# Optimization experiments

Hardware: AMD Instinct MI355X
Metric: run time of the kernel (lower is better)

## Reference

```python
import jax, jax.numpy as jnp
import numpy as np

NUM_EXPERTS = 8
TOP_K = 2
TOKENS = 4096
HIDDEN = 1024
INTER = 2048
INIT_STD = 0.01  # nnx.initializers.normal() default stddev


def setup_inputs() -> dict:
    key = jax.random.key(0)
    k1, k2, k3, k4, k5 = jax.random.split(key, 5)
    return {
        "inputs": jax.random.normal(k1, (TOKENS, HIDDEN), jnp.float32),
        "router_logits": jax.random.normal(k2, (TOKENS, NUM_EXPERTS), jnp.float32),
        "wi_0": jax.random.normal(k3, (NUM_EXPERTS, HIDDEN, INTER), jnp.float32) * INIT_STD,
        "wi_1": jax.random.normal(k4, (NUM_EXPERTS, HIDDEN, INTER), jnp.float32) * INIT_STD,
        "wo": jax.random.normal(k5, (NUM_EXPERTS, INTER, HIDDEN), jnp.float32) * INIT_STD,
    }


def reference(inputs, router_logits, wi_0, wi_1, wo):
    T, H = inputs.shape
    # --- top-k routing ---
    top_k_logits, top_k_indices = jax.lax.top_k(router_logits, TOP_K)  # [T, k]
    w = jax.nn.softmax(top_k_logits, axis=-1)
    w = w / jnp.sum(w, axis=-1, keepdims=True)  # (redundant renorm, kept faithful)
    # --- permute: sort token-expert pairs by expert id ---
    flat_experts = top_k_indices.reshape(-1)          # [T*k]
    sort_idx = jnp.argsort(flat_experts)              # stable sort -> token order within group
    token_idx = sort_idx // TOP_K                     # source token of each sorted slot
    x = inputs[token_idx]                             # [T*k, H] gathered/permuted tokens
    group_sizes = jnp.bincount(flat_experts, length=NUM_EXPERTS).astype(jnp.int32)
    # --- grouped (ragged) GEMM experts: silu(x@wi_0) * (x@wi_1) @ wo ---
    h0 = jax.lax.ragged_dot(x, wi_0, group_sizes, preferred_element_type=jnp.float32)
    h1 = jax.lax.ragged_dot(x, wi_1, group_sizes, preferred_element_type=jnp.float32)
    act = jax.nn.silu(h0) * h1                        # [T*k, INTER]
    y = jax.lax.ragged_dot(act, wo, group_sizes, preferred_element_type=jnp.float32)  # [T*k, H]
    # --- unpermute + weighted combine over top-k ---
    unsort = jnp.argsort(sort_idx)
    y = y[unsort].reshape(T, TOP_K, H)
    return jnp.sum(y * w[..., None], axis=1)          # [T, H]
```

## Files before the change

kernel.cpp:

```cpp
#include <hip/hip_runtime.h>
#include <hip/hip_bf16.h>

#define T_TOKENS 4096
#define HID 1024
#define INTER 2048
#define NEXP 8
#define TOPK 2
#define RTOT (T_TOKENS * TOPK)
#define BMT 128
#define BN 128
#define MAXT (RTOT / BMT + NEXP)

typedef __attribute__((ext_vector_type(8))) short bf16x8;
typedef __attribute__((ext_vector_type(4))) float f32x4;

typedef __attribute__((address_space(1))) const unsigned int gu32;
typedef __attribute__((address_space(3))) unsigned int lu32;

__device__ __forceinline__ void gl16(const void* g, void* l) {
  __builtin_amdgcn_global_load_lds((gu32*)g, (lu32*)l, 16, 0, 0);
}

__device__ __forceinline__ unsigned f2bf(float f) {
  union { float f; unsigned u; } v; v.f = f;
  unsigned u = v.u;
  return (u + 0x7FFFu + ((u >> 16) & 1u)) >> 16;
}

__device__ __forceinline__ float bf2f(unsigned short s) {
  union { unsigned u; float f; } v; v.u = ((unsigned)s) << 16;
  return v.f;
}

__device__ __forceinline__ int swz(int row, int kb) {
  return row * 128 + (kb ^ ((row & 7) << 4));
}

__device__ __forceinline__ void phase_barrier() {
  asm volatile("" ::: "memory");
  __builtin_amdgcn_s_barrier();
  asm volatile("" ::: "memory");
}

__device__ __forceinline__ int psig(int kap) { return kap ^ ((kap & 1) << 2); }

__global__ __launch_bounds__(1024)
void k_routing(const float* __restrict__ logits, int* ntiles,
               int* te2, int* tr02, int* tcnt2,
               float* pw, int* rows, float* rw, int* slotOf) {
  __shared__ int cnt[NEXP];
  __shared__ int cur[NEXP];
  const int tid = threadIdx.x;
  if (tid < NEXP) cnt[tid] = 0;
  __syncthreads();

  int myE[4][2];
  float myW[4][2];
#pragma unroll
  for (int j = 0; j < 4; ++j) {
    int t = j * 1024 + tid;
    float l[NEXP];
#pragma unroll
    for (int i = 0; i < NEXP; ++i) l[i] = logits[t * NEXP + i];
    int i0 = 0; float b0 = l[0];
#pragma unroll
    for (int i = 1; i < NEXP; ++i) if (l[i] > b0) { b0 = l[i]; i0 = i; }
    int i1 = -1; float b1 = -1e30f;
#pragma unroll
    for (int i = 0; i < NEXP; ++i) if (i != i0 && l[i] > b1) { b1 = l[i]; i1 = i; }
    float e = __expf(b1 - b0);
    float w0 = 1.f / (1.f + e);
    float w1 = e / (1.f + e);
    myE[j][0] = i0; myE[j][1] = i1;
    myW[j][0] = w0; myW[j][1] = w1;
    pw[2 * t] = w0; pw[2 * t + 1] = w1;
#pragma unroll
    for (int ex = 0; ex < NEXP; ++ex) {
      int c = __popcll(__ballot(i0 == ex)) + __popcll(__ballot(i1 == ex));
      if ((tid & 63) == 0 && c) atomicAdd(&cnt[ex], c);
    }
  }
  __syncthreads();

  if (tid == 0) {
    int off = 0, nm = 0;
    for (int e = 0; e < NEXP; ++e) {
      int c = cnt[e];
      cur[e] = off;
      for (int m0 = 0; m0 < c; m0 += BMT) {
        te2[nm] = e; tr02[nm] = off + m0; tcnt2[nm] = min(BMT, c - m0); ++nm;
      }
      off += c;
    }
    ntiles[1] = nm;
  }
  __syncthreads();

#pragma unroll
  for (int j = 0; j < 4; ++j) {
    int t = j * 1024 + tid;
#pragma unroll
    for (int k = 0; k < TOPK; ++k) {
      int e = myE[j][k];
      int s = atomicAdd(&cur[e], 1);
      rows[s] = t;
      rw[s] = myW[j][k];
      slotOf[2 * t + k] = s;
    }
  }
}

__global__ __launch_bounds__(256)
void k_prep1(const float* __restrict__ X, unsigned short* __restrict__ Xb,
             const float* __restrict__ W0, const float* __restrict__ W1,
             unsigned short* __restrict__ T0, unsigned short* __restrict__ T1) {
  int bid = blockIdx.x;
  const int tid = threadIdx.x;
  if (bid < 1024) {
    int base = bid * 1024 + tid;
#pragma unroll
    for (int j = 0; j < 4; ++j) {
      int i = base + j * 256;
      float4 v = *(const float4*)(X + (size_t)i * 4);
      uint2 p;
      p.x = f2bf(v.x) | (f2bf(v.y) << 16);
      p.y = f2bf(v.z) | (f2bf(v.w) << 16);
      *(uint2*)(Xb + (size_t)i * 4) = p;
    }
    return;
  }
  bid -= 1024;
  const int w = bid >> 11;
  const int r = bid & 2047;
  const float* W = (w == 0) ? W0 : W1;
  unsigned short* T = (w == 0) ? T0 : T1;
  const int kt = r & 15, nt = (r >> 4) & 15, e = r >> 8;
  __shared__ float ls[64 * 128];
  const float* src = W + (size_t)e * HID * INTER + (size_t)(kt * 64) * INTER + nt * 128;
#pragma unroll
  for (int t = 0; t < 8; ++t) {
    int u = t * 256 + tid;
    int k = u >> 5, n4 = u & 31;
    float4 v = *(const float4*)(src + (size_t)k * INTER + n4 * 4);
    *(float4*)(ls + k * 128 + ((n4 ^ psig(k >> 3)) << 2)) = v;
  }
  __syncthreads();
  unsigned short* dst = T + (((size_t)e * 16 + nt) * 16 + kt) * 8192;
#pragma unroll
  for (int t = 0; t < 4; ++t) {
    int v = t * 256 + tid;
    int kt2 = v >> 9, n = (v >> 2) & 127, sw = v & 3;
    int kc = kt2 * 4 + (sw ^ ((n >> 1) & 3));
    const float* col = ls + (size_t)(kc * 8) * 128 +
                       (((n >> 2) ^ psig(kc)) << 2) + (n & 3);
    unsigned b[8];
#pragma unroll
    for (int i = 0; i < 8; ++i) b[i] = f2bf(col[i * 128]);
    uint4 q;
    q.x = b[0] | (b[1] << 16); q.y = b[2] | (b[3] << 16);
    q.z = b[4] | (b[5] << 16); q.w = b[6] | (b[7] << 16);
    *(uint4*)(dst + (size_t)v * 8) = q;
  }
}

__global__ __launch_bounds__(512, 4)
void k_gemm1w(const unsigned short* __restrict__ Xb,
              const unsigned short* __restrict__ WT0,
              const unsigned short* __restrict__ WT1,
              const float* __restrict__ WO,
              unsigned short* __restrict__ WTo,
              const int* __restrict__ ntiles, const int* __restrict__ te2,
              const int* __restrict__ tr02, const int* __restrict__ tcnt2,
              const int* __restrict__ rows,
              unsigned short* __restrict__ act) {
  const int ty = blockIdx.y;
  const int nt = blockIdx.x;
  const int tid = threadIdx.x;
  __shared__ __align__(16) unsigned char sm[49152];

  if (ty >= MAXT) {
    const int r = (ty - MAXT) * 16 + nt;
    const int kt = r & 31, ntt = (r >> 5) & 7, e = r >> 8;
    float* ls = (float*)sm;
    const float* src = WO + (size_t)e * INTER * HID + (size_t)(kt * 64) * HID + ntt * 128;
#pragma unroll
    for (int t = 0; t < 4; ++t) {
      int u = t * 512 + tid;
      int k = u >> 5, n4 = u & 31;
      float4 v = *(const float4*)(src + (size_t)k * HID + n4 * 4);
      *(float4*)(ls + k * 128 + ((n4 ^ psig(k >> 3)) << 2)) = v;
    }
    __syncthreads();
    unsigned short* dst = WTo + (((size_t)e * 8 + ntt) * 32 + kt) * 8192;
#pragma unroll
    for (int t = 0; t < 2; ++t) {
      int v = t * 512 + tid;
      int kt2 = v >> 9, n = (v >> 2) & 127, sw = v & 3;
      int kc = kt2 * 4 + (sw ^ ((n >> 1) & 3));
      const float* col = ls + (size_t)(kc * 8) * 128 +
                         (((n >> 2) ^ psig(kc)) << 2) + (n & 3);
      unsigned b[8];
#pragma unroll
      for (int i = 0; i < 8; ++i) b[i] = f2bf(col[i * 128]);
      uint4 q;
      q.x = b[0] | (b[1] << 16); q.y = b[2] | (b[3] << 16);
      q.z = b[4] | (b[5] << 16); q.w = b[6] | (b[7] << 16);
      *(uint4*)(dst + (size_t)v * 8) = q;
    }
    return;
  }

  if (ty >= ntiles[1]) return;
  const int e = te2[ty], row0 = tr02[ty], mcnt = tcnt2[ty];
  const int n0 = nt * BN;
  const int lane = tid & 63, wv = tid >> 6;
  const int mh = wv >> 2, nq = wv & 3;
  const int l15 = lane & 15, sl = lane >> 4;

  const int am = tid >> 2;
  const int atok = rows[row0 + (am < mcnt ? am : mcnt - 1)];
  const int askc = ((tid & 3) ^ ((tid >> 3) & 3)) * 8;
  const unsigned short* B0t = WT0 + ((size_t)e * 16 + nt) * 32 * 4096;
  const unsigned short* B1t = WT1 + ((size_t)e * 16 + nt) * 32 * 4096;

  int aoff[4], boff[2];
#pragma unroll
  for (int f = 0; f < 4; ++f) {
    int m = mh * 64 + f * 16 + l15;
    aoff[f] = m * 64 + ((sl ^ ((m >> 1) & 3)) << 4);
  }
#pragma unroll
  for (int g = 0; g < 2; ++g) {
    int n = nq * 32 + g * 16 + l15;
    boff[g] = n * 64 + ((sl ^ ((n >> 1) & 3)) << 4);
  }

  f32x4 acc0[4][2], acc1[4][2];
  const f32x4 zz = {0.f, 0.f, 0.f, 0.f};
#pragma unroll
  for (int f = 0; f < 4; ++f)
#pragma unroll
    for (int g = 0; g < 2; ++g) { acc0[f][g] = zz; acc1[f][g] = zz; }

  const int NT_K = HID / 32;

  gl16(Xb + (size_t)atok * HID + askc, sm + tid * 16);
  gl16(B0t + (size_t)tid * 8, sm + 8192 + tid * 16);
  gl16(B1t + (size_t)tid * 8, sm + 16384 + tid * 16);

  for (int t = 0; t < NT_K; ++t) {
    unsigned char* cur = sm + (t & 1) * 24576;
    unsigned char* nxt = sm + ((t + 1) & 1) * 24576;
    const int tn = (t + 1 < NT_K) ? (t + 1) : (NT_K - 1);

    gl16(Xb + (size_t)atok * HID + tn * 32 + askc, nxt + tid * 16);
    gl16(B0t + (size_t)tn * 4096 + tid * 8, nxt + 8192 + tid * 16);
    gl16(B1t + (size_t)tn * 4096 + tid * 8, nxt + 16384 + tid * 16);
    asm volatile("s_waitcnt vmcnt(3)" ::: "memory");
    __builtin_amdgcn_sched_barrier(0);
    phase_barrier();

    bf16x8 aA[4], b0q[2], b1q[2];
#pragma unroll
    for (int g = 0; g < 2; ++g) {
      b0q[g] = *(const bf16x8*)(cur + 8192 + boff[g]);
      b1q[g] = *(const bf16x8*)(cur + 16384 + boff[g]);
    }
#pragma unroll
    for (int f = 0; f < 4; ++f) aA[f] = *(const bf16x8*)(cur + aoff[f]);
    __builtin_amdgcn_s_setprio(1);
#pragma unroll
    for (int f = 0; f < 4; ++f)
#pragma unroll
      for (int g = 0; g < 2; ++g) {
        acc0[f][g] = __builtin_amdgcn_mfma_f32_16x16x32_bf16(aA[f], b0q[g], acc0[f][g], 0, 0, 0);
        acc1[f][g] = __builtin_amdgcn_mfma_f32_16x16x32_bf16(aA[f], b1q[g], acc1[f][g], 0, 0, 0);
      }
    __builtin_amdgcn_s_setprio(0);
    phase_barrier();
  }

#pragma unroll
  for (int f = 0; f < 4; ++f) {
#pragma unroll
    for (int r = 0; r < 4; ++r) {
      int m = mh * 64 + f * 16 + sl * 4 + r;
      if (m >= mcnt) continue;
      size_t base = (size_t)(row0 + m) * INTER + n0 + nq * 32 + l15;
#pragma unroll
      for (int g = 0; g < 2; ++g) {
        float h0 = acc0[f][g][r];
        float h1 = acc1[f][g][r];
        float s = h0 / (1.f + __expf(-h0));
        act[base + g * 16] = (unsigned short)f2bf(s * h1);
      }
    }
  }
}

__global__ __launch_bounds__(256, 4)
void k_gemm2n(const unsigned short* __restrict__ act,
              const unsigned short* __restrict__ WTo,
              const int* __restrict__ ntiles, const int* __restrict__ te2,
              const int* __restrict__ tr02, const int* __restrict__ tcnt2,
              unsigned short* __restrict__ y) {
  const int ty = blockIdx.y;
  if (ty >= ntiles[1]) return;
  const int e = te2[ty], row0 = tr02[ty], mcnt = tcnt2[ty];
  const int nt = blockIdx.x, n0 = nt * BN;
  const int tid = threadIdx.x, lane = tid & 63, wv = tid >> 6;
  const int wr = wv >> 1, wc = wv & 1;
  const int l15 = lane & 15, sl = lane >> 4;

  __shared__ __align__(16) unsigned char sm[32768];

  const int am0 = tid >> 2, am1 = 64 + (tid >> 2);
  const int ar0 = row0 + (am0 < mcnt ? am0 : mcnt - 1);
  const int ar1 = row0 + (am1 < mcnt ? am1 : mcnt - 1);
  const int askc = ((tid & 3) ^ ((tid >> 3) & 3)) * 8;
  const unsigned short* Bt = WTo + ((size_t)e * 8 + nt) * 64 * 4096;

  int aoff[4], boff[4];
#pragma unroll
  for (int f = 0; f < 4; ++f) {
    int m = wr * 64 + f * 16 + l15;
    aoff[f] = m * 64 + ((sl ^ ((m >> 1) & 3)) << 4);
    int n = wc * 64 + f * 16 + l15;
    boff[f] = n * 64 + ((sl ^ ((n >> 1) & 3)) << 4);
  }

  f32x4 acc[4][4];
  const f32x4 zz = {0.f, 0.f, 0.f, 0.f};
#pragma unroll
  for (int i = 0; i < 4; ++i)
#pragma unroll
    for (int j = 0; j < 4; ++j) acc[i][j] = zz;

  const int NT_K = INTER / 32;

  gl16(act + (size_t)ar0 * INTER + askc, sm + tid * 16);
  gl16(act + (size_t)ar1 * INTER + askc, sm + (256 + tid) * 16);
  gl16(Bt + (size_t)tid * 8, sm + 8192 + tid * 16);
  gl16(Bt + (size_t)(256 + tid) * 8, sm + 8192 + (256 + tid) * 16);

  for (int t = 0; t < NT_K; ++t) {
    unsigned char* cur = sm + (t & 1) * 16384;
    unsigned char* nxt = sm + ((t + 1) & 1) * 16384;
    const int tn = (t + 1 < NT_K) ? (t + 1) : (NT_K - 1);

    gl16(act + (size_t)ar0 * INTER + tn * 32 + askc, nxt + tid * 16);
    gl16(act + (size_t)ar1 * INTER + tn * 32 + askc, nxt + (256 + tid) * 16);
    gl16(Bt + (size_t)tn * 4096 + tid * 8, nxt + 8192 + tid * 16);
    gl16(Bt + ((size_t)tn * 4096 + 2048) + tid * 8, nxt + 8192 + (256 + tid) * 16);
    asm volatile("s_waitcnt vmcnt(4)" ::: "memory");
    __builtin_amdgcn_sched_barrier(0);
    phase_barrier();

    bf16x8 af[4], bb[4];
#pragma unroll
    for (int f = 0; f < 4; ++f) {
      af[f] = *(const bf16x8*)(cur + aoff[f]);
      bb[f] = *(const bf16x8*)(cur + 8192 + boff[f]);
    }
    __builtin_amdgcn_s_setprio(1);
#pragma unroll
    for (int mf = 0; mf < 4; ++mf)
#pragma unroll
      for (int nf = 0; nf < 4; ++nf)
        acc[mf][nf] = __builtin_amdgcn_mfma_f32_16x16x32_bf16(af[mf], bb[nf], acc[mf][nf], 0, 0, 0);
    __builtin_amdgcn_s_setprio(0);
    phase_barrier();
  }

#pragma unroll
  for (int mf = 0; mf < 4; ++mf) {
#pragma unroll
    for (int r = 0; r < 4; ++r) {
      int m = wr * 64 + mf * 16 + sl * 4 + r;
      if (m >= mcnt) continue;
      unsigned short* yp = y + (size_t)(row0 + m) * HID + n0 + wc * 64 + l15;
#pragma unroll
      for (int nf = 0; nf < 4; ++nf)
        yp[nf * 16] = (unsigned short)f2bf(acc[mf][nf][r]);
    }
  }
}

__global__ void k_combine(const unsigned short* __restrict__ y,
                          const float* __restrict__ pw,
                          const int* __restrict__ slotOf,
                          float* __restrict__ out) {
  int idx = blockIdx.x * blockDim.x + threadIdx.x;
  int t = idx >> 7, hc = (idx & 127) * 8;
  int s0 = slotOf[2 * t], s1 = slotOf[2 * t + 1];
  float w0 = pw[2 * t], w1 = pw[2 * t + 1];
  uint4 a = *(const uint4*)(y + (size_t)s0 * HID + hc);
  uint4 b = *(const uint4*)(y + (size_t)s1 * HID + hc);
  float o[8];
  const unsigned* ap = (const unsigned*)&a;
  const unsigned* bp = (const unsigned*)&b;
#pragma unroll
  for (int i = 0; i < 4; ++i) {
    o[2 * i]     = w0 * bf2f((unsigned short)(ap[i] & 0xFFFF)) + w1 * bf2f((unsigned short)(bp[i] & 0xFFFF));
    o[2 * i + 1] = w0 * bf2f((unsigned short)(ap[i] >> 16))    + w1 * bf2f((unsigned short)(bp[i] >> 16));
  }
  float* op = out + (size_t)t * HID + hc;
  *(float4*)op = make_float4(o[0], o[1], o[2], o[3]);
  *(float4*)(op + 4) = make_float4(o[4], o[5], o[6], o[7]);
}

__global__ __launch_bounds__(256, 2)
void k_gemm1_fb(const float* __restrict__ X, const float* __restrict__ W0,
                const float* __restrict__ W1, const int* __restrict__ ntiles,
                const int* __restrict__ te2, const int* __restrict__ tr02,
                const int* __restrict__ tcnt2, const int* __restrict__ rows,
                unsigned short* __restrict__ act) {
  const int ty = blockIdx.y;
  if (ty >= ntiles[1]) return;
  const int e = te2[ty], row0 = tr02[ty], mcnt = tcnt2[ty];
  const int n0 = blockIdx.x * BN;
  const int tid = threadIdx.x;
  const int lane = tid & 63, wv = tid >> 6;
  const int wr = wv >> 1, wc = wv & 1;

  __shared__ unsigned char smf[49152];
  unsigned char* As = smf;
  unsigned char* B0s = smf + 16384;
  unsigned char* B1s = smf + 32768;

  int atok[8];
#pragma unroll
  for (int j = 0; j < 8; ++j) {
    int m = (j * 256 + tid) >> 4;
    atok[j] = (m < mcnt) ? rows[row0 + m] : -1;
  }
  const int bnb = (tid & 7) | ((tid >> 7) << 6);
  const int bc = (tid >> 3) & 15;

  f32x4 acc0[4][4], acc1[4][4];
  const f32x4 zz = {0.f, 0.f, 0.f, 0.f};
#pragma unroll
  for (int i = 0; i < 4; ++i)
#pragma unroll
    for (int j = 0; j < 4; ++j) { acc0[i][j] = zz; acc1[i][j] = zz; }

  const float* W0e = W0 + (size_t)e * HID * INTER + n0;
  const float* W1e = W1 + (size_t)e * HID * INTER + n0;

  for (int k0 = 0; k0 < HID; k0 += 64) {
#pragma unroll
    for (int j = 0; j < 8; ++j) {
      int c = j * 256 + tid;
      int m = c >> 4, ch = c & 15;
      float4 v = make_float4(0.f, 0.f, 0.f, 0.f);
      int tok = atok[j];
      if (tok >= 0) v = *(const float4*)(X + (size_t)tok * HID + k0 + 4 * ch);
      uint2 p;
      p.x = f2bf(v.x) | (f2bf(v.y) << 16);
      p.y = f2bf(v.z) | (f2bf(v.w) << 16);
      *(uint2*)(As + swz(m, 8 * ch)) = p;
    }
#pragma unroll
    for (int j = 0; j < 8; ++j) {
      int n = bnb | (j << 3);
      const float* p0 = W0e + (size_t)(k0 + 4 * bc) * INTER + n;
      float a0 = p0[0], a1 = p0[INTER], a2 = p0[2 * INTER], a3 = p0[3 * INTER];
      uint2 q;
      q.x = f2bf(a0) | (f2bf(a1) << 16);
      q.y = f2bf(a2) | (f2bf(a3) << 16);
      *(uint2*)(B0s + swz(n, 8 * bc)) = q;
      const float* p1 = W1e + (size_t)(k0 + 4 * bc) * INTER + n;
      a0 = p1[0]; a1 = p1[INTER]; a2 = p1[2 * INTER]; a3 = p1[3 * INTER];
      q.x = f2bf(a0) | (f2bf(a1) << 16);
      q.y = f2bf(a2) | (f2bf(a3) << 16);
      *(uint2*)(B1s + swz(n, 8 * bc)) = q;
    }
    __syncthreads();
#pragma unroll
    for (int kq = 0; kq < 2; ++kq) {
      int kb = kq * 64 + 16 * (lane >> 4);
      bf16x8 a[4], b0[4], b1[4];
#pragma unroll
      for (int f = 0; f < 4; ++f) {
        int m = wr * 64 + f * 16 + (lane & 15);
        a[f] = *(const bf16x8*)(As + swz(m, kb));
        int n = wc * 64 + f * 16 + (lane & 15);
        b0[f] = *(const bf16x8*)(B0s + swz(n, kb));
        b1[f] = *(const bf16x8*)(B1s + swz(n, kb));
      }
#pragma unroll
      for (int mf = 0; mf < 4; ++mf)
#pragma unroll
        for (int nf = 0; nf < 4; ++nf) {
          acc0[mf][nf] = __builtin_amdgcn_mfma_f32_16x16x32_bf16(a[mf], b0[nf], acc0[mf][nf], 0, 0, 0);
          acc1[mf][nf] = __builtin_amdgcn_mfma_f32_16x16x32_bf16(a[mf], b1[nf], acc1[mf][nf], 0, 0, 0);
        }
    }
    __syncthreads();
  }
#pragma unroll
  for (int mf = 0; mf < 4; ++mf) {
#pragma unroll
    for (int r = 0; r < 4; ++r) {
      int m = wr * 64 + mf * 16 + (lane >> 4) * 4 + r;
      if (m >= mcnt) continue;
      size_t rowbase = (size_t)(row0 + m) * INTER + n0 + wc * 64 + (lane & 15);
#pragma unroll
      for (int nf = 0; nf < 4; ++nf) {
        float h0 = acc0[mf][nf][r];
        float h1 = acc1[mf][nf][r];
        float s = h0 / (1.f + __expf(-h0));
        act[rowbase + nf * 16] = (unsigned short)f2bf(s * h1);
      }
    }
  }
}

__global__ __launch_bounds__(256, 2)
void k_gemm2_fb(const unsigned short* __restrict__ act, const float* __restrict__ WO,
                const int* __restrict__ ntiles, const int* __restrict__ te2,
                const int* __restrict__ tr02, const int* __restrict__ tcnt2,
                const int* __restrict__ rows, const float* __restrict__ rw,
                float* __restrict__ out) {
  const int ty = blockIdx.y;
  if (ty >= ntiles[1]) return;
  const int e = te2[ty], row0 = tr02[ty], mcnt = tcnt2[ty];
  const int n0 = blockIdx.x * BN;
  const int tid = threadIdx.x;
  const int lane = tid & 63, wv = tid >> 6;
  const int wr = wv >> 1, wc = wv & 1;

  __shared__ unsigned char smf[32768];
  unsigned char* As = smf;
  unsigned char* Bs = smf + 16384;

  const int bnb = (tid & 7) | ((tid >> 7) << 6);
  const int bc = (tid >> 3) & 15;

  f32x4 acc[4][4];
  const f32x4 zz = {0.f, 0.f, 0.f, 0.f};
#pragma unroll
  for (int i = 0; i < 4; ++i)
#pragma unroll
    for (int j = 0; j < 4; ++j) acc[i][j] = zz;

  const float* We = WO + (size_t)e * INTER * HID + n0;

  for (int k0 = 0; k0 < INTER; k0 += 64) {
#pragma unroll
    for (int j = 0; j < 4; ++j) {
      int u = j * 256 + tid;
      int m = u >> 3, ch = u & 7;
      uint4 v = make_uint4(0u, 0u, 0u, 0u);
      if (m < mcnt)
        v = *(const uint4*)(act + (size_t)(row0 + m) * INTER + k0 + 8 * ch);
      *(uint4*)(As + swz(m, 16 * ch)) = v;
    }
#pragma unroll
    for (int j = 0; j < 8; ++j) {
      int n = bnb | (j << 3);
      const float* p = We + (size_t)(k0 + 4 * bc) * HID + n;
      float a0 = p[0], a1 = p[HID], a2 = p[2 * HID], a3 = p[3 * HID];
      uint2 q;
      q.x = f2bf(a0) | (f2bf(a1) << 16);
      q.y = f2bf(a2) | (f2bf(a3) << 16);
      *(uint2*)(Bs + swz(n, 8 * bc)) = q;
    }
    __syncthreads();
#pragma unroll
    for (int kq = 0; kq < 2; ++kq) {
      int kb = kq * 64 + 16 * (lane >> 4);
      bf16x8 a[4], b[4];
#pragma unroll
      for (int f = 0; f < 4; ++f) {
        int m = wr * 64 + f * 16 + (lane & 15);
        a[f] = *(const bf16x8*)(As + swz(m, kb));
        int n = wc * 64 + f * 16 + (lane & 15);
        b[f] = *(const bf16x8*)(Bs + swz(n, kb));
      }
#pragma unroll
      for (int mf = 0; mf < 4; ++mf)
#pragma unroll
        for (int nf = 0; nf < 4; ++nf)
          acc[mf][nf] = __builtin_amdgcn_mfma_f32_16x16x32_bf16(a[mf], b[nf], acc[mf][nf], 0, 0, 0);
    }
    __syncthreads();
  }
#pragma unroll
  for (int mf = 0; mf < 4; ++mf) {
#pragma unroll
    for (int r = 0; r < 4; ++r) {
      int m = wr * 64 + mf * 16 + (lane >> 4) * 4 + r;
      if (m >= mcnt) continue;
      int tok = rows[row0 + m];
      float w = rw[row0 + m];
      float* op = out + (size_t)tok * HID + n0 + wc * 64 + (lane & 15);
#pragma unroll
      for (int nf = 0; nf < 4; ++nf)
        atomicAdd(op + nf * 16, w * acc[mf][nf][r]);
    }
  }
}

extern "C" void kernel_launch(void* const* d_in, const int* in_sizes, int n_in,
                              void* d_out, int out_size, void* d_ws, size_t ws_size,
                              hipStream_t stream) {
  const float* X  = (const float*)d_in[0];
  const float* RL = (const float*)d_in[1];
  const float* W0 = (const float*)d_in[2];
  const float* W1 = (const float*)d_in[3];
  const float* WOp = (const float*)d_in[4];
  float* out = (float*)d_out;

  char* ws = (char*)d_ws;
  int* ntiles  = (int*)(ws + 128);
  int* te2     = (int*)(ws + 2048);
  int* tr02    = (int*)(ws + 2560);
  int* tcnt2   = (int*)(ws + 3072);
  float* pw    = (float*)(ws + 8192 + 32768);
  int* rows    = (int*)(ws + 8192 + 65536);
  float* rw    = (float*)(ws + 8192 + 98304);
  int* slotOf  = (int*)(ws + 8192 + 131072);

  const bool big = ws_size >= ((size_t)145 << 20);

  k_routing<<<1, 1024, 0, stream>>>(RL, ntiles, te2, tr02, tcnt2, pw, rows, rw, slotOf);

  if (big) {
    unsigned short* Xb  = (unsigned short*)(ws + ((size_t)1 << 20));
    unsigned short* act = (unsigned short*)(ws + ((size_t)16 << 20));
    unsigned short* WT0 = (unsigned short*)(ws + ((size_t)48 << 20));
    unsigned short* WT1 = (unsigned short*)(ws + ((size_t)80 << 20));
    unsigned short* WTo = (unsigned short*)(ws + ((size_t)112 << 20));
    unsigned short* y   = (unsigned short*)(ws + ((size_t)48 << 20));

    k_prep1<<<5120, 256, 0, stream>>>(X, Xb, W0, W1, WT0, WT1);

    k_gemm1w<<<dim3(INTER / BN, MAXT + 128), 512, 0, stream>>>(
        Xb, WT0, WT1, WOp, WTo, ntiles, te2, tr02, tcnt2, rows, act);
    k_gemm2n<<<dim3(HID / BN, MAXT), 256, 0, stream>>>(act, WTo, ntiles, te2, tr02, tcnt2, y);
    k_combine<<<(T_TOKENS * HID / 8) / 256, 256, 0, stream>>>(y, pw, slotOf, out);
  } else {
    unsigned short* act = (unsigned short*)(ws + ((size_t)1 << 20));
    hipMemsetAsync(d_out, 0, (size_t)out_size * sizeof(float), stream);
    k_gemm1_fb<<<dim3(INTER / BN, MAXT), 256, 0, stream>>>(X, W0, W1, ntiles, te2, tr02, tcnt2, rows, act);
    k_gemm2_fb<<<dim3(HID / BN, MAXT), 256, 0, stream>>>(act, WOp, ntiles, te2, tr02, tcnt2, rows, rw, out);
  }
}
```

Before: 215.4 us.

## Fold routing into weight-prep kernel and reorder weight-transpose block indexing

Removes the separate single-block routing launch on the fast path by running routing as block 0 of the weight/input conversion kernel, so it overlaps with the bf16 conversion work. Routing recomputes top-k in its second pass instead of holding it in registers. The block-to-tile mapping in the weight transposes is swapped so consecutive blocks walk along N instead of K, which changes the DRAM access locality. Routing in a single 256-thread block now processes 16 tokens per thread and could become the tail of the prep kernel.

Measured after the change: 211.5 us. About the same (-1.8%).

```diff
diff --git a/kernel.cpp b/kernel.cpp
--- a/kernel.cpp
+++ b/kernel.cpp
@@ -53,9 +53,6 @@
   const int tid = threadIdx.x;
   if (tid < NEXP) cnt[tid] = 0;
   __syncthreads();
-
-  int myE[4][2];
-  float myW[4][2];
 #pragma unroll
   for (int j = 0; j < 4; ++j) {
     int t = j * 1024 + tid;
@@ -71,8 +68,6 @@
     float e = __expf(b1 - b0);
     float w0 = 1.f / (1.f + e);
     float w1 = e / (1.f + e);
-    myE[j][0] = i0; myE[j][1] = i1;
-    myW[j][0] = w0; myW[j][1] = w1;
     pw[2 * t] = w0; pw[2 * t + 1] = w1;
 #pragma unroll
     for (int ex = 0; ex < NEXP; ++ex) {
@@ -81,7 +76,6 @@
     }
   }
   __syncthreads();
-
   if (tid == 0) {
     int off = 0, nm = 0;
     for (int e = 0; e < NEXP; ++e) {
@@ -95,29 +89,110 @@
     ntiles[1] = nm;
   }
   __syncthreads();
-
 #pragma unroll
   for (int j = 0; j < 4; ++j) {
     int t = j * 1024 + tid;
+    float l[NEXP];
+#pragma unroll
+    for (int i = 0; i < NEXP; ++i) l[i] = logits[t * NEXP + i];
+    int i0 = 0; float b0 = l[0];
+#pragma unroll
+    for (int i = 1; i < NEXP; ++i) if (l[i] > b0) { b0 = l[i]; i0 = i; }
+    int i1 = -1; float b1 = -1e30f;
+#pragma unroll
+    for (int i = 0; i < NEXP; ++i) if (i != i0 && l[i] > b1) { b1 = l[i]; i1 = i; }
+    float e = __expf(b1 - b0);
+    float ww[2] = {1.f / (1.f + e), e / (1.f + e)};
+    int ee[2] = {i0, i1};
 #pragma unroll
     for (int k = 0; k < TOPK; ++k) {
-      int e = myE[j][k];
-      int s = atomicAdd(&cur[e], 1);
+      int s = atomicAdd(&cur[ee[k]], 1);
       rows[s] = t;
-      rw[s] = myW[j][k];
+      rw[s] = ww[k];
       slotOf[2 * t + k] = s;
     }
   }
 }
 
 __global__ __launch_bounds__(256)
-void k_prep1(const float* __restrict__ X, unsigned short* __restrict__ Xb,
-             const float* __restrict__ W0, const float* __restrict__ W1,
-             unsigned short* __restrict__ T0, unsigned short* __restrict__ T1) {
+void k_prep1r(const float* __restrict__ X, unsigned short* __restrict__ Xb,
+              const float* __restrict__ W0, const float* __restrict__ W1,
+              unsigned short* __restrict__ T0, unsigned short* __restrict__ T1,
+              const float* __restrict__ logits, int* ntiles,
+              int* te2, int* tr02, int* tcnt2,
+              float* pw, int* rows, float* rw, int* slotOf) {
   int bid = blockIdx.x;
   const int tid = threadIdx.x;
-  if (bid < 1024) {
-    int base = bid * 1024 + tid;
+
+  if (bid == 0) {
+    __shared__ int cnt[NEXP];
+    __shared__ int cur[NEXP];
+    if (tid < NEXP) cnt[tid] = 0;
+    __syncthreads();
+#pragma unroll
+    for (int j = 0; j < 16; ++j) {
+      int t = j * 256 + tid;
+      float l[NEXP];
+#pragma unroll
+      for (int i = 0; i < NEXP; ++i) l[i] = logits[t * NEXP + i];
+      int i0 = 0; float b0 = l[0];
+#pragma unroll
+      for (int i = 1; i < NEXP; ++i) if (l[i] > b0) { b0 = l[i]; i0 = i; }
+      int i1 = -1; float b1 = -1e30f;
+#pragma unroll
+      for (int i = 0; i < NEXP; ++i) if (i != i0 && l[i] > b1) { b1 = l[i]; i1 = i; }
+      float e = __expf(b1 - b0);
+      float w0 = 1.f / (1.f + e);
+      pw[2 * t] = w0; pw[2 * t + 1] = 1.f - w0;
+#pragma unroll
+      for (int ex = 0; ex < NEXP; ++ex) {
+        int c = __popcll(__ballot(i0 == ex)) + __popcll(__ballot(i1 == ex));
+        if ((tid & 63) == 0 && c) atomicAdd(&cnt[ex], c);
+      }
+    }
+    __syncthreads();
+    if (tid == 0) {
+      int off = 0, nm = 0;
+      for (int e = 0; e < NEXP; ++e) {
+        int c = cnt[e];
+        cur[e] = off;
+        for (int m0 = 0; m0 < c; m0 += BMT) {
+          te2[nm] = e; tr02[nm] = off + m0; tcnt2[nm] = min(BMT, c - m0); ++nm;
+        }
+        off += c;
+      }
+      ntiles[1] = nm;
+    }
+    __syncthreads();
+#pragma unroll
+    for (int j = 0; j < 16; ++j) {
+      int t = j * 256 + tid;
+      float l[NEXP];
+#pragma unroll
+      for (int i = 0; i < NEXP; ++i) l[i] = logits[t * NEXP + i];
+      int i0 = 0; float b0 = l[0];
+#pragma unroll
+      for (int i = 1; i < NEXP; ++i) if (l[i] > b0) { b0 = l[i]; i0 = i; }
+      int i1 = -1; float b1 = -1e30f;
+#pragma unroll
+      for (int i = 0; i < NEXP; ++i) if (i != i0 && l[i] > b1) { b1 = l[i]; i1 = i; }
+      float e = __expf(b1 - b0);
+      float ww0 = 1.f / (1.f + e);
+      int ee[2] = {i0, i1};
+      float ww[2] = {ww0, 1.f - ww0};
+#pragma unroll
+      for (int k = 0; k < TOPK; ++k) {
+        int s = atomicAdd(&cur[ee[k]], 1);
+        rows[s] = t;
+        rw[s] = ww[k];
+        slotOf[2 * t + k] = s;
+      }
+    }
+    return;
+  }
+
+  if (bid < 1025) {
+    int base = (bid - 1) * 1024 + tid;
 #pragma unroll
     for (int j = 0; j < 4; ++j) {
       int i = base + j * 256;
@@ -129,12 +204,12 @@
     }
     return;
   }
-  bid -= 1024;
+  bid -= 1025;
   const int w = bid >> 11;
   const int r = bid & 2047;
   const float* W = (w == 0) ? W0 : W1;
   unsigned short* T = (w == 0) ? T0 : T1;
-  const int kt = r & 15, nt = (r >> 4) & 15, e = r >> 8;
+  const int nt = r & 15, kt = (r >> 4) & 15, e = r >> 8;
   __shared__ float ls[64 * 128];
   const float* src = W + (size_t)e * HID * INTER + (size_t)(kt * 64) * INTER + nt * 128;
 #pragma unroll
@@ -180,7 +255,7 @@
 
   if (ty >= MAXT) {
     const int r = (ty - MAXT) * 16 + nt;
-    const int kt = r & 31, ntt = (r >> 5) & 7, e = r >> 8;
+    const int ntt = r & 7, kt = (r >> 3) & 31, e = r >> 8;
     float* ls = (float*)sm;
     const float* src = WO + (size_t)e * INTER * HID + (size_t)(kt * 64) * HID + ntt * 128;
 #pragma unroll
@@ -624,8 +699,6 @@
 
   const bool big = ws_size >= ((size_t)145 << 20);
 
-  k_routing<<<1, 1024, 0, stream>>>(RL, ntiles, te2, tr02, tcnt2, pw, rows, rw, slotOf);
-
   if (big) {
     unsigned short* Xb  = (unsigned short*)(ws + ((size_t)1 << 20));
     unsigned short* act = (unsigned short*)(ws + ((size_t)16 << 20));
@@ -634,7 +707,9 @@
     unsigned short* WTo = (unsigned short*)(ws + ((size_t)112 << 20));
     unsigned short* y   = (unsigned short*)(ws + ((size_t)48 << 20));
 
-    k_prep1<<<5120, 256, 0, stream>>>(X, Xb, W0, W1, WT0, WT1);
+    k_prep1r<<<5121, 256, 0, stream>>>(X, Xb, W0, W1, WT0, WT1,
+                                       RL, ntiles, te2, tr02, tcnt2,
+                                       pw, rows, rw, slotOf);
 
     k_gemm1w<<<dim3(INTER / BN, MAXT + 128), 512, 0, stream>>>(
         Xb, WT0, WT1, WOp, WTo, ntiles, te2, tr02, tcnt2, rows, act);
@@ -643,6 +718,7 @@
   } else {
     unsigned short* act = (unsigned short*)(ws + ((size_t)1 << 20));
     hipMemsetAsync(d_out, 0, (size_t)out_size * sizeof(float), stream);
+    k_routing<<<1, 1024, 0, stream>>>(RL, ntiles, te2, tr02, tcnt2, pw, rows, rw, slotOf);
     k_gemm1_fb<<<dim3(INTER / BN, MAXT), 256, 0, stream>>>(X, W0, W1, ntiles, te2, tr02, tcnt2, rows, act);
     k_gemm2_fb<<<dim3(HID / BN, MAXT), 256, 0, stream>>>(act, WOp, ntiles, te2, tr02, tcnt2, rows, rw, out);
   }
```
